# Performance work log

Hardware: AMD Instinct MI355X
Metric: run time of the kernel (lower is better)

The kernel has to match this reference:

```python
import jax, jax.numpy as jnp
import numpy as np

VOCAB, EMB, HID = 32000, 128, 256
B, T = 512, 512


def setup_inputs() -> dict:
    key = jax.random.key(0)
    ks = jax.random.split(key, 6)
    x = jax.random.randint(ks[0], (B, T), 0, VOCAB, dtype=jnp.int64) if jax.config.jax_enable_x64 else jax.random.randint(ks[0], (B, T), 0, VOCAB, dtype=jnp.int32)
    s_e = 1.0 / np.sqrt(HID)
    emb = jax.random.normal(ks[1], (VOCAB, EMB), dtype=jnp.float32)
    W_ih = jax.random.uniform(ks[2], (3 * HID, EMB), dtype=jnp.float32, minval=-s_e, maxval=s_e)
    W_hh = jax.random.uniform(ks[3], (3 * HID, HID), dtype=jnp.float32, minval=-s_e, maxval=s_e)
    b_ih = jax.random.uniform(ks[4], (3 * HID,), dtype=jnp.float32, minval=-s_e, maxval=s_e)
    b_hh = jax.random.uniform(ks[5], (3 * HID,), dtype=jnp.float32, minval=-s_e, maxval=s_e)
    return {"x": x, "emb": emb, "W_ih": W_ih, "W_hh": W_hh, "b_ih": b_ih, "b_hh": b_hh}


def reference(x, emb, W_ih, W_hh, b_ih, b_hh):
    # in_len = x.shape[0] per original code (loops x[:, t, :] for t in range(x.shape[0]))
    in_len = x.shape[0]
    H = W_hh.shape[1]
    xe = emb[x]                                   # [B, T, E]
    xs = jnp.swapaxes(xe[:, :in_len, :], 0, 1)    # [in_len, B, E]
    # precompute input-side gate projections for all timesteps (one big GEMM)
    gi = jnp.einsum('tbe,ge->tbg', xs, W_ih) + b_ih   # [in_len, B, 3H]

    def step(h, gi_t):
        gh = h @ W_hh.T + b_hh                    # [B, 3H]
        i_r, i_z, i_n = gi_t[:, :H], gi_t[:, H:2*H], gi_t[:, 2*H:]
        h_r, h_z, h_n = gh[:, :H], gh[:, H:2*H], gh[:, 2*H:]
        r = jax.nn.sigmoid(i_r + h_r)
        z = jax.nn.sigmoid(i_z + h_z)
        n = jnp.tanh(i_n + r * h_n)
        h_new = (1.0 - z) * n + z * h
        return h_new, None

    h0 = jnp.zeros((x.shape[0], H), dtype=emb.dtype)  # batch = x.shape[0]
    hT, _ = jax.lax.scan(step, h0, gi)
    return hT
```

## Files before the change

kernel.cpp:

```cpp
#include <hip/hip_runtime.h>


typedef unsigned short ushort_t;
typedef __attribute__((ext_vector_type(8))) short short8;
typedef __attribute__((ext_vector_type(4))) float float4_;
typedef __attribute__((ext_vector_type(4))) unsigned short ushort4_;
typedef __attribute__((ext_vector_type(2))) unsigned int uint2_;
typedef __attribute__((ext_vector_type(4))) int int4_;

#define VOCAB 32000
#define EMB 128
#define HID 256
#define G3 768
#define TT 512
#define HB 98304
#define XB 114688

__device__ __forceinline__ float b2f(ushort_t u) {
  return __uint_as_float(((unsigned)u) << 16);
}
__device__ __forceinline__ ushort_t f2b(float f) {
  unsigned u = __float_as_uint(f);
  return (ushort_t)((u + 0x7FFFu + ((u >> 16) & 1u)) >> 16);
}
__device__ __forceinline__ short8 ld8(const ushort_t* p) { return *(const short8*)p; }
__device__ __forceinline__ void gld_lds16(const void* g, void* l) {
  __builtin_amdgcn_global_load_lds((const __attribute__((address_space(1))) void*)g,
                                   (__attribute__((address_space(3))) void*)l, 16, 0, 0);
}
__device__ __forceinline__ int gi_byte(int bl, int c) {
  return ((bl * 1536) + c) ^ ((bl & 7) << 4);
}

__global__ void cvt_bf16_k(const float* __restrict__ s, ushort_t* __restrict__ d, int n4) {
  int i = blockIdx.x * blockDim.x + threadIdx.x;
  int stride = gridDim.x * blockDim.x;
  for (; i < n4; i += stride) {
    float4_ v = ((const float4_*)s)[i];
    ushort4_ o;
    o.x = f2b(v.x); o.y = f2b(v.y); o.z = f2b(v.z); o.w = f2b(v.w);
    ((ushort4_*)d)[i] = o;
  }
}

__global__ __launch_bounds__(256) void tbl_gemm(
    const ushort_t* __restrict__ emb16, const ushort_t* __restrict__ Wih16,
    const float* __restrict__ bih, const float* __restrict__ bhh,
    char* __restrict__ tb_out) {
  __shared__ float cbs[G3];
  __shared__ alignas(16) char img[16 * 1552];
  const int tid = threadIdx.x;
  for (int i = tid; i < G3; i += 256) cbs[i] = bih[i] + (i < 512 ? bhh[i] : 0.f);
  const int lane = tid & 63, w = tid >> 6;
  const int bl = lane & 15, kg = lane >> 4;
  const int v0 = blockIdx.x * 16;

  short8 bfr[4];
#pragma unroll
  for (int kt = 0; kt < 4; ++kt)
    bfr[kt] = ld8(emb16 + (size_t)(v0 + bl) * EMB + kt * 32 + kg * 8);
  __syncthreads();

#pragma unroll 1
  for (int mi = 0; mi < 12; ++mi) {
    int mt = w * 12 + mi;
    short8 af[4];
#pragma unroll
    for (int kt = 0; kt < 4; ++kt)
      af[kt] = ld8(Wih16 + (mt * 16 + bl) * EMB + kt * 32 + kg * 8);
    float4_ acc = {0.f, 0.f, 0.f, 0.f};
#pragma unroll
    for (int kt = 0; kt < 4; ++kt)
      acc = __builtin_amdgcn_mfma_f32_16x16x32_bf16(af[kt], bfr[kt], acc, 0, 0, 0);
    int g0 = mt * 16 + kg * 4;
    ushort4_ o;
#pragma unroll
    for (int r = 0; r < 4; ++r) o[r] = f2b(acc[r] + cbs[g0 + r]);
    *(ushort4_*)(img + bl * 1552 + mt * 32 + kg * 8) = o;
  }
  __syncthreads();

#pragma unroll
  for (int c = 0; c < 6; ++c) {
    int p = c * 4096 + tid * 16;
    int q = p >> 9;
    int row = (q * 21846) >> 16;
    int off = p - row * 1536;
    float4_ v = *(const float4_*)(img + row * 1552 + off);
    *(float4_*)(tb_out + (size_t)(v0 + row) * 1536 + off) = v;
  }
}

__global__ __launch_bounds__(512, 2) void gru_rec(
    const ushort_t* __restrict__ Whh16, const char* __restrict__ tbl,
    const float* __restrict__ bhh, const int* __restrict__ x,
    float* __restrict__ out) {
  __shared__ alignas(16) char smem[147456];

  const int tid = threadIdx.x, lane = tid & 63, w = tid >> 6;
  const int bl = lane & 15, kg = lane >> 4;
  const int b0 = blockIdx.x * 16;

  {
    const int4_* xs = (const int4_*)(x + (size_t)b0 * TT);
    int4_* xd = (int4_*)(smem + XB);
#pragma unroll
    for (int i = 0; i < 4; ++i) xd[tid + i * 512] = xs[tid + i * 512];
    int4_ z4 = {0, 0, 0, 0};
    *(int4_*)(smem + HB + tid * 16) = z4;
  }
  __syncthreads();

  short8 wf[2][3][8];
#pragma unroll
  for (int i = 0; i < 2; ++i)
#pragma unroll
    for (int q = 0; q < 3; ++q) {
      int g = (w + 8 * i + 16 * q) * 16 + bl;
#pragma unroll
      for (int kt = 0; kt < 8; ++kt)
        wf[i][q][kt] = ld8(Whh16 + (size_t)g * HID + kt * 32 + kg * 8);
    }

  float4_ bhn[2];
  float hreg[2][4];
#pragma unroll
  for (int i = 0; i < 2; ++i) {
    bhn[i] = *(const float4_*)&bhh[512 + (w + 8 * i) * 16 + kg * 4];
#pragma unroll
    for (int r = 0; r < 4; ++r) hreg[i][r] = 0.f;
  }

  const int s0 = ((2 * w) & 7) << 4, s1 = ((2 * w + 1) & 7) << 4;
  const unsigned inv0 = (unsigned)((lane * 16) ^ s0);
  const unsigned inv1 = (lane < 32) ? (unsigned)((1024 + lane * 16) ^ s0)
                                    : (unsigned)((lane * 16 - 512) ^ s1);
  const unsigned inv2 = (unsigned)((512 + lane * 16) ^ s1);
  const int* xtA = (const int*)(smem + XB) + (2 * w) * TT;
  const int* xtB = (const int*)(smem + XB) + (2 * w + 1) * TT;

  asm volatile("s_waitcnt vmcnt(0)" ::: "memory");

#pragma unroll
  for (int tau = 0; tau < 3; ++tau) {
    int tokA = xtA[tau], tokB = xtB[tau];
    const char* pA = tbl + (unsigned)tokA * 1536u;
    const char* pB = tbl + (unsigned)tokB * 1536u;
    const char* pM = (lane < 32) ? pA : pB;
    char* d0 = smem + tau * 24576 + w * 3072;
    gld_lds16(pA + inv0, d0);
    gld_lds16(pM + inv1, d0 + 1024);
    gld_lds16(pB + inv2, d0 + 2048);
  }

#pragma unroll 1
  for (int t = 0; t < TT; ++t) {
    int rem = TT - 1 - t;
    if (rem >= 2)
      asm volatile("s_waitcnt vmcnt(6) lgkmcnt(0)" ::: "memory");
    else if (rem == 1)
      asm volatile("s_waitcnt vmcnt(3) lgkmcnt(0)" ::: "memory");
    else
      asm volatile("s_waitcnt vmcnt(0) lgkmcnt(0)" ::: "memory");
    __builtin_amdgcn_s_barrier();
    __builtin_amdgcn_sched_barrier(0);

    const int slot = t & 3, cur = t & 1, nxt = cur ^ 1;
    if (t + 3 < TT) {
      int tokA = xtA[t + 3], tokB = xtB[t + 3];
      const char* pA = tbl + (unsigned)tokA * 1536u;
      const char* pB = tbl + (unsigned)tokB * 1536u;
      const char* pM = (lane < 32) ? pA : pB;
      char* d0 = smem + ((t + 3) & 3) * 24576 + w * 3072;
      gld_lds16(pA + inv0, d0);
      gld_lds16(pM + inv1, d0 + 1024);
      gld_lds16(pB + inv2, d0 + 2048);
    }

    const char* gtile = smem + slot * 24576;

    float4_ acc[2][3];
#pragma unroll
    for (int i = 0; i < 2; ++i) {
#pragma unroll
      for (int q = 0; q < 2; ++q) {
        int byte8 = gi_byte(bl, 32 * (w + 8 * i + 16 * q) + 8 * kg);
        ushort4_ v = *(const ushort4_*)(gtile + byte8);
#pragma unroll
        for (int r = 0; r < 4; ++r) acc[i][q][r] = b2f(v[r]);
      }
      acc[i][2] = bhn[i];
    }

#pragma unroll
    for (int kt = 0; kt < 8; ++kt) {
      int byteoff = ((bl * 512) + kt * 64 + kg * 16) ^ ((bl & 7) << 4);
      short8 bf = *(const short8*)(smem + HB + cur * 8192 + byteoff);
#pragma unroll
      for (int i = 0; i < 2; ++i)
#pragma unroll
        for (int q = 0; q < 3; ++q)
          acc[i][q] = __builtin_amdgcn_mfma_f32_16x16x32_bf16(wf[i][q][kt], bf, acc[i][q], 0, 0, 0);
    }

#pragma unroll
    for (int i = 0; i < 2; ++i) {
      int byte8n = gi_byte(bl, 32 * (32 + w + 8 * i) + 8 * kg);
      ushort4_ gv = *(const ushort4_*)(gtile + byte8n);
#pragma unroll
      for (int r = 0; r < 4; ++r) {
        float rr = __builtin_amdgcn_rcpf(1.f + __expf(-acc[i][0][r]));
        float zz = __builtin_amdgcn_rcpf(1.f + __expf(-acc[i][1][r]));
        float y = b2f(gv[r]) + rr * acc[i][2][r];
        float nn = 1.f - 2.f * __builtin_amdgcn_rcpf(1.f + __expf(2.f * y));
        hreg[i][r] = (1.f - zz) * nn + zz * hreg[i][r];
      }
      int byte0 = (bl * 512 + ((w + 8 * i) * 16 + kg * 4) * 2) ^ ((bl & 7) << 4);
      uint2_ hv;
      hv.x = (unsigned)f2b(hreg[i][0]) | ((unsigned)f2b(hreg[i][1]) << 16);
      hv.y = (unsigned)f2b(hreg[i][2]) | ((unsigned)f2b(hreg[i][3]) << 16);
      *(uint2_*)(smem + HB + nxt * 8192 + byte0) = hv;
    }
  }

#pragma unroll
  for (int i = 0; i < 2; ++i) {
    float4_ v = {hreg[i][0], hreg[i][1], hreg[i][2], hreg[i][3]};
    *(float4_*)&out[(size_t)(b0 + bl) * HID + (w + 8 * i) * 16 + kg * 4] = v;
  }
}

extern "C" void kernel_launch(void* const* d_in, const int* in_sizes, int n_in,
                              void* d_out, int out_size, void* d_ws, size_t ws_size,
                              hipStream_t stream) {
  const int* x = (const int*)d_in[0];
  const float* emb = (const float*)d_in[1];
  const float* Wih = (const float*)d_in[2];
  const float* Whh = (const float*)d_in[3];
  const float* bih = (const float*)d_in[4];
  const float* bhh = (const float*)d_in[5];
  float* out = (float*)d_out;

  char* ws = (char*)d_ws;
  ushort_t* emb16 = (ushort_t*)ws;
  ushort_t* Wih16 = (ushort_t*)(ws + 8192000);
  ushort_t* Whh16 = (ushort_t*)(ws + 8388608);
  char* tbl = ws + 8781824;

  cvt_bf16_k<<<1024, 256, 0, stream>>>(emb, emb16, (VOCAB * EMB) / 4);
  cvt_bf16_k<<<96, 256, 0, stream>>>(Wih, Wih16, (G3 * EMB) / 4);
  cvt_bf16_k<<<192, 256, 0, stream>>>(Whh, Whh16, (G3 * HID) / 4);
  tbl_gemm<<<2000, 256, 0, stream>>>(emb16, Wih16, bih, bhh, tbl);
  gru_rec<<<32, 512, 0, stream>>>(Whh16, tbl, bhh, x, out);
}
```

Baseline: 1.361 ms.

## Fuse input projection into recurrence via producer blocks and flag-synchronized ring buffer

Replaces the full-vocabulary projection table GEMM and separate recurrence kernel with one persistent launch. 224 producer blocks compute per-timestep input gate projections for the actual tokens and write them into a global ring buffer. Each slot is signalled with atomic flags, and recurrence blocks spin-wait on those flags. This removes the 32000-row table precompute and overlaps the projection with the sequential recurrence. It relies on co-residency of all 256 blocks and adds spin-wait and progress-counter backpressure overhead.

```diff
diff --git a/kernel.cpp b/kernel.cpp
--- a/kernel.cpp
+++ b/kernel.cpp
@@ -13,8 +13,14 @@
 #define HID 256
 #define G3 768
 #define TT 512
-#define HB 98304
-#define XB 114688
+#define SLOT 786432
+#define BLK_BYTES 24576
+#define RING_T 256
+#define FLAGS_OFF 8781824
+#define PROG_OFF 8782336
+#define GI_OFF 8785920
+#define NPROD 224
+#define NITEM 4096
 
 __device__ __forceinline__ float b2f(ushort_t u) {
   return __uint_as_float(((unsigned)u) << 16);
@@ -30,6 +36,13 @@
 }
 __device__ __forceinline__ int gi_byte(int bl, int c) {
   return ((bl * 1536) + c) ^ ((bl & 7) << 4);
+}
+__device__ __forceinline__ void wait_item(const unsigned* flags, int item) {
+  const unsigned bit = 1u << (item & 31);
+  const unsigned* wp = flags + (item >> 5);
+  while (!(__hip_atomic_load(wp, __ATOMIC_RELAXED, __HIP_MEMORY_SCOPE_AGENT) & bit))
+    __builtin_amdgcn_s_sleep(8);
+  __builtin_amdgcn_fence(__ATOMIC_ACQUIRE, "agent");
 }
 
 __global__ void cvt_bf16_k(const float* __restrict__ s, ushort_t* __restrict__ d, int n4) {
@@ -43,71 +56,101 @@
   }
 }
 
-__global__ __launch_bounds__(256) void tbl_gemm(
-    const ushort_t* __restrict__ emb16, const ushort_t* __restrict__ Wih16,
+__global__ __launch_bounds__(512, 1) void gru_fused(
+    const int* __restrict__ x, const ushort_t* __restrict__ emb16,
+    const ushort_t* __restrict__ Wih16, const ushort_t* __restrict__ Whh16,
     const float* __restrict__ bih, const float* __restrict__ bhh,
-    char* __restrict__ tb_out) {
-  __shared__ float cbs[G3];
-  __shared__ alignas(16) char img[16 * 1552];
-  const int tid = threadIdx.x;
-  for (int i = tid; i < G3; i += 256) cbs[i] = bih[i] + (i < 512 ? bhh[i] : 0.f);
-  const int lane = tid & 63, w = tid >> 6;
-  const int bl = lane & 15, kg = lane >> 4;
-  const int v0 = blockIdx.x * 16;
-
-  short8 bfr[4];
-#pragma unroll
-  for (int kt = 0; kt < 4; ++kt)
-    bfr[kt] = ld8(emb16 + (size_t)(v0 + bl) * EMB + kt * 32 + kg * 8);
-  __syncthreads();
-
-#pragma unroll 1
-  for (int mi = 0; mi < 12; ++mi) {
-    int mt = w * 12 + mi;
-    short8 af[4];
-#pragma unroll
-    for (int kt = 0; kt < 4; ++kt)
-      af[kt] = ld8(Wih16 + (mt * 16 + bl) * EMB + kt * 32 + kg * 8);
-    float4_ acc = {0.f, 0.f, 0.f, 0.f};
-#pragma unroll
-    for (int kt = 0; kt < 4; ++kt)
-      acc = __builtin_amdgcn_mfma_f32_16x16x32_bf16(af[kt], bfr[kt], acc, 0, 0, 0);
-    int g0 = mt * 16 + kg * 4;
-    ushort4_ o;
-#pragma unroll
-    for (int r = 0; r < 4; ++r) o[r] = f2b(acc[r] + cbs[g0 + r]);
-    *(ushort4_*)(img + bl * 1552 + mt * 32 + kg * 8) = o;
-  }
-  __syncthreads();
-
-#pragma unroll
-  for (int c = 0; c < 6; ++c) {
-    int p = c * 4096 + tid * 16;
-    int q = p >> 9;
-    int row = (q * 21846) >> 16;
-    int off = p - row * 1536;
-    float4_ v = *(const float4_*)(img + row * 1552 + off);
-    *(float4_*)(tb_out + (size_t)(v0 + row) * 1536 + off) = v;
-  }
-}
-
-__global__ __launch_bounds__(512, 2) void gru_rec(
-    const ushort_t* __restrict__ Whh16, const char* __restrict__ tbl,
-    const float* __restrict__ bhh, const int* __restrict__ x,
-    float* __restrict__ out) {
-  __shared__ alignas(16) char smem[147456];
-
+    char* __restrict__ gi, unsigned* __restrict__ flags,
+    int* __restrict__ progress, float* __restrict__ out) {
+  __shared__ alignas(16) char smem[117760];
   const int tid = threadIdx.x, lane = tid & 63, w = tid >> 6;
   const int bl = lane & 15, kg = lane >> 4;
-  const int b0 = blockIdx.x * 16;
+  const int s16 = (bl & 7) << 4;
+
+  if (blockIdx.x >= 32) {
+    const int pid = blockIdx.x - 32;
+    char* img = smem;
+    char* xe = smem + 98304;
+    float* cb = (float*)(smem + 114688);
+    for (int i = tid; i < G3; i += 512) cb[i] = bih[i] + (i < 512 ? bhh[i] : 0.f);
+    __syncthreads();
+
+#pragma unroll 1
+    for (int it = pid; it < NITEM; it += NPROD) {
+      const int tq = it >> 5, blk = it & 31, t0 = tq * 4;
+#pragma unroll
+      for (int gg = 0; gg < 2; ++gg) {
+        int g = 2 * w + gg;
+        int row = g * 4 + (lane >> 4);
+        int tok = x[(blk * 16 + (row & 15)) * TT + t0 + (row >> 4)];
+        const char* src = (const char*)emb16 + (size_t)((unsigned)tok) * 256u +
+                          ((((unsigned)lane & 15u) << 4) ^ (((unsigned)row & 15u) << 4));
+        gld_lds16(src, xe + g * 1024);
+      }
+      asm volatile("s_waitcnt vmcnt(0)" ::: "memory");
+      __syncthreads();
+      short8 bfr[4][4];
+#pragma unroll
+      for (int t = 0; t < 4; ++t)
+#pragma unroll
+        for (int kt = 0; kt < 4; ++kt)
+          bfr[t][kt] = *(const short8*)(xe + (t * 16 + bl) * 256 +
+                                        ((kt * 64 + kg * 16) ^ (bl << 4)));
+#pragma unroll 1
+      for (int mi = 0; mi < 6; ++mi) {
+        int mt = w * 6 + mi;
+        short8 af[4];
+#pragma unroll
+        for (int kt = 0; kt < 4; ++kt)
+          af[kt] = ld8(Wih16 + (mt * 16 + bl) * EMB + kt * 32 + kg * 8);
+        float4_ z4 = {0.f, 0.f, 0.f, 0.f};
+        float4_ acc[4] = {z4, z4, z4, z4};
+#pragma unroll
+        for (int kt = 0; kt < 4; ++kt)
+#pragma unroll
+          for (int t = 0; t < 4; ++t)
+            acc[t] = __builtin_amdgcn_mfma_f32_16x16x32_bf16(af[kt], bfr[t][kt], acc[t], 0, 0, 0);
+        float4_ cbv = *(const float4_*)(cb + mt * 16 + kg * 4);
+        int db = (bl * 1536 + 32 * mt + 8 * kg) ^ s16;
+#pragma unroll
+        for (int t = 0; t < 4; ++t) {
+          ushort4_ o;
+#pragma unroll
+          for (int r = 0; r < 4; ++r) o[r] = f2b(acc[t][r] + cbv[r]);
+          *(ushort4_*)(img + t * 24576 + db) = o;
+        }
+      }
+      __syncthreads();
+      if (tq >= 64) {
+        int need = 4 * tq - 252;
+        while (__hip_atomic_load(&progress[blk], __ATOMIC_RELAXED,
+                                 __HIP_MEMORY_SCOPE_AGENT) < need)
+          __builtin_amdgcn_s_sleep(16);
+        __builtin_amdgcn_fence(__ATOMIC_ACQUIRE, "agent");
+      }
+      char* dstb = gi + (size_t)(t0 & (RING_T - 1)) * SLOT + (size_t)blk * BLK_BYTES;
+#pragma unroll
+      for (int t = 0; t < 4; ++t)
+#pragma unroll
+        for (int ii = 0; ii < 3; ++ii) {
+          float4_ v = *(const float4_*)(img + t * 24576 + tid * 48 + ii * 16);
+          *(float4_*)(dstb + (size_t)t * SLOT + tid * 48 + ii * 16) = v;
+        }
+      asm volatile("s_waitcnt vmcnt(0)" ::: "memory");
+      __syncthreads();
+      if (tid == 0)
+        __hip_atomic_fetch_or(&flags[it >> 5], 1u << (it & 31),
+                              __ATOMIC_RELEASE, __HIP_MEMORY_SCOPE_AGENT);
+    }
+    return;
+  }
+
+  const int bx = blockIdx.x;
+  const int b0 = bx * 16;
 
   {
-    const int4_* xs = (const int4_*)(x + (size_t)b0 * TT);
-    int4_* xd = (int4_*)(smem + XB);
-#pragma unroll
-    for (int i = 0; i < 4; ++i) xd[tid + i * 512] = xs[tid + i * 512];
     int4_ z4 = {0, 0, 0, 0};
-    *(int4_*)(smem + HB + tid * 16) = z4;
+    *(int4_*)(smem + 98304 + tid * 16) = z4;
   }
   __syncthreads();
 
@@ -131,26 +174,17 @@
     for (int r = 0; r < 4; ++r) hreg[i][r] = 0.f;
   }
 
-  const int s0 = ((2 * w) & 7) << 4, s1 = ((2 * w + 1) & 7) << 4;
-  const unsigned inv0 = (unsigned)((lane * 16) ^ s0);
-  const unsigned inv1 = (lane < 32) ? (unsigned)((1024 + lane * 16) ^ s0)
-                                    : (unsigned)((lane * 16 - 512) ^ s1);
-  const unsigned inv2 = (unsigned)((512 + lane * 16) ^ s1);
-  const int* xtA = (const int*)(smem + XB) + (2 * w) * TT;
-  const int* xtB = (const int*)(smem + XB) + (2 * w + 1) * TT;
-
-  asm volatile("s_waitcnt vmcnt(0)" ::: "memory");
-
+  asm volatile("s_waitcnt vmcnt(0) lgkmcnt(0)" ::: "memory");
+  __builtin_amdgcn_s_barrier();
+  __builtin_amdgcn_sched_barrier(0);
+
+  wait_item(flags, bx);
 #pragma unroll
   for (int tau = 0; tau < 3; ++tau) {
-    int tokA = xtA[tau], tokB = xtB[tau];
-    const char* pA = tbl + (unsigned)tokA * 1536u;
-    const char* pB = tbl + (unsigned)tokB * 1536u;
-    const char* pM = (lane < 32) ? pA : pB;
-    char* d0 = smem + tau * 24576 + w * 3072;
-    gld_lds16(pA + inv0, d0);
-    gld_lds16(pM + inv1, d0 + 1024);
-    gld_lds16(pB + inv2, d0 + 2048);
+    const char* src = gi + (size_t)tau * SLOT + (size_t)bx * BLK_BYTES + (w * 3) * 1024 + lane * 16;
+    char* dst = smem + tau * 24576 + (w * 3) * 1024;
+#pragma unroll
+    for (int ii = 0; ii < 3; ++ii) gld_lds16(src + ii * 1024, dst + ii * 1024);
   }
 
 #pragma unroll 1
@@ -165,16 +199,18 @@
     __builtin_amdgcn_s_barrier();
     __builtin_amdgcn_sched_barrier(0);
 
+    if (((t & 15) == 0) && tid == 0)
+      __hip_atomic_fetch_max(&progress[bx], t + 1, __ATOMIC_RELAXED,
+                             __HIP_MEMORY_SCOPE_AGENT);
+
     const int slot = t & 3, cur = t & 1, nxt = cur ^ 1;
     if (t + 3 < TT) {
-      int tokA = xtA[t + 3], tokB = xtB[t + 3];
-      const char* pA = tbl + (unsigned)tokA * 1536u;
-      const char* pB = tbl + (unsigned)tokB * 1536u;
-      const char* pM = (lane < 32) ? pA : pB;
-      char* d0 = smem + ((t + 3) & 3) * 24576 + w * 3072;
-      gld_lds16(pA + inv0, d0);
-      gld_lds16(pM + inv1, d0 + 1024);
-      gld_lds16(pB + inv2, d0 + 2048);
+      if (((t + 3) & 3) == 0) wait_item(flags, ((t + 3) >> 2) * 32 + bx);
+      const char* src = gi + (size_t)((t + 3) & (RING_T - 1)) * SLOT +
+                        (size_t)bx * BLK_BYTES + (w * 3) * 1024 + lane * 16;
+      char* dst = smem + ((t + 3) & 3) * 24576 + (w * 3) * 1024;
+#pragma unroll
+      for (int ii = 0; ii < 3; ++ii) gld_lds16(src + ii * 1024, dst + ii * 1024);
     }
 
     const char* gtile = smem + slot * 24576;
@@ -194,8 +230,8 @@
 
 #pragma unroll
     for (int kt = 0; kt < 8; ++kt) {
-      int byteoff = ((bl * 512) + kt * 64 + kg * 16) ^ ((bl & 7) << 4);
-      short8 bf = *(const short8*)(smem + HB + cur * 8192 + byteoff);
+      int byteoff = ((bl * 512) + kt * 64 + kg * 16) ^ s16;
+      short8 bf = *(const short8*)(smem + 98304 + cur * 8192 + byteoff);
 #pragma unroll
       for (int i = 0; i < 2; ++i)
 #pragma unroll
@@ -215,11 +251,11 @@
         float nn = 1.f - 2.f * __builtin_amdgcn_rcpf(1.f + __expf(2.f * y));
         hreg[i][r] = (1.f - zz) * nn + zz * hreg[i][r];
       }
-      int byte0 = (bl * 512 + ((w + 8 * i) * 16 + kg * 4) * 2) ^ ((bl & 7) << 4);
+      int byte0 = (bl * 512 + ((w + 8 * i) * 16 + kg * 4) * 2) ^ s16;
       uint2_ hv;
       hv.x = (unsigned)f2b(hreg[i][0]) | ((unsigned)f2b(hreg[i][1]) << 16);
       hv.y = (unsigned)f2b(hreg[i][2]) | ((unsigned)f2b(hreg[i][3]) << 16);
-      *(uint2_*)(smem + HB + nxt * 8192 + byte0) = hv;
+      *(uint2_*)(smem + 98304 + nxt * 8192 + byte0) = hv;
     }
   }
 
@@ -245,11 +281,13 @@
   ushort_t* emb16 = (ushort_t*)ws;
   ushort_t* Wih16 = (ushort_t*)(ws + 8192000);
   ushort_t* Whh16 = (ushort_t*)(ws + 8388608);
-  char* tbl = ws + 8781824;
+  unsigned* flags = (unsigned*)(ws + FLAGS_OFF);
+  int* progress = (int*)(ws + PROG_OFF);
+  char* gi = ws + GI_OFF;
 
   cvt_bf16_k<<<1024, 256, 0, stream>>>(emb, emb16, (VOCAB * EMB) / 4);
   cvt_bf16_k<<<96, 256, 0, stream>>>(Wih, Wih16, (G3 * EMB) / 4);
   cvt_bf16_k<<<192, 256, 0, stream>>>(Whh, Whh16, (G3 * HID) / 4);
-  tbl_gemm<<<2000, 256, 0, stream>>>(emb16, Wih16, bih, bhh, tbl);
-  gru_rec<<<32, 512, 0, stream>>>(Whh16, tbl, bhh, x, out);
-}
+  hipMemsetAsync(ws + FLAGS_OFF, 0, 1024, stream);
+  gru_fused<<<256, 512, 0, stream>>>(x, emb16, Wih16, Whh16, bih, bhh, gi, flags, progress, out);
+}
```

Result: slower. 1.696 ms (+24.6%).
